# Performance work log

Hardware: AMD Instinct MI355X
Metric: run time of the kernel (lower is better)

## Reference

```python
import jax, jax.numpy as jnp
import numpy as np

N_NODES = 50000
N_EDGES = 800000
IN_DIM = 128
HID = 256
HEADS = 4
OUT_DIM = 128
NEG_SLOPE = 0.2


def gat_conv(x, src, dst, W, a_src, a_dst, b, heads, out_ch):
    """PyG-style GATConv: per-edge attention + segment softmax over dst."""
    N = x.shape[0]
    h = (x @ W).reshape(N, heads, out_ch)              # [N,H,C]
    alph_s = jnp.einsum('nhc,hc->nh', h, a_src)        # [N,H]
    alph_d = jnp.einsum('nhc,hc->nh', h, a_dst)        # [N,H]
    e = jax.nn.leaky_relu(alph_s[src] + alph_d[dst], NEG_SLOPE)  # [E,H]
    m = jax.lax.stop_gradient(jax.ops.segment_max(e, dst, num_segments=N))
    ex = jnp.exp(e - m[dst])
    s = jax.ops.segment_sum(ex, dst, num_segments=N)
    alpha = ex / (s[dst] + 1e-16)                      # [E,H]
    out = jax.ops.segment_sum(h[src] * alpha[:, :, None], dst, num_segments=N)
    return out.reshape(N, heads * out_ch) + b


def setup_inputs() -> dict:
    key = jax.random.key(0)
    ks = jax.random.split(key, 12)
    x = jax.random.normal(ks[0], (N_NODES, IN_DIM), dtype=jnp.float32)
    edge_index = jax.random.randint(ks[1], (2, N_EDGES), 0, N_NODES, dtype=jnp.int64)
    c1 = HID // HEADS  # 64
    sc1 = 1.0 / np.sqrt(IN_DIM)
    sc2 = 1.0 / np.sqrt(HID)
    W1 = jax.random.normal(ks[2], (IN_DIM, HID), dtype=jnp.float32) * sc1
    a1_src = jax.random.normal(ks[3], (HEADS, c1), dtype=jnp.float32) * sc1
    a1_dst = jax.random.normal(ks[4], (HEADS, c1), dtype=jnp.float32) * sc1
    b1 = jnp.zeros((HID,), dtype=jnp.float32)
    W2 = jax.random.normal(ks[5], (HID, OUT_DIM), dtype=jnp.float32) * sc2
    a2_src = jax.random.normal(ks[6], (1, OUT_DIM), dtype=jnp.float32) * sc2
    a2_dst = jax.random.normal(ks[7], (1, OUT_DIM), dtype=jnp.float32) * sc2
    b2 = jnp.zeros((OUT_DIM,), dtype=jnp.float32)
    return {"x": x, "edge_index": edge_index, "W1": W1, "a1_src": a1_src,
            "a1_dst": a1_dst, "b1": b1, "W2": W2, "a2_src": a2_src,
            "a2_dst": a2_dst, "b2": b2}


def reference(x, edge_index, W1, a1_src, a1_dst, b1, W2, a2_src, a2_dst, b2):
    N = x.shape[0]
    loops = jnp.arange(N, dtype=edge_index.dtype)
    # PyG default add_self_loops=True
    src = jnp.concatenate([edge_index[0], loops])
    dst = jnp.concatenate([edge_index[1], loops])
    h = jax.nn.relu(gat_conv(x, src, dst, W1, a1_src, a1_dst, b1, HEADS, HID // HEADS))
    # dropout is identity in eval mode
    return gat_conv(h, src, dst, W2, a2_src, a2_dst, b2, 1, OUT_DIM)
```

## Files before the change

kernel.cpp:

```cpp
#include <hip/hip_runtime.h>
#include <math.h>

#define NEG_SLOPE 0.2f
#define SLOTS 64
#define ECAP 63
#define NBMAX 391
#define BCAP 2432

typedef __attribute__((ext_vector_type(8))) short bf16x8;
typedef __attribute__((ext_vector_type(4))) float f32x4;
typedef __attribute__((ext_vector_type(2))) float f32x2;

__device__ __forceinline__ float lrelu(float t) {
    return t > 0.f ? t : NEG_SLOPE * t;
}
__device__ __forceinline__ unsigned short f2bf(float f) {
    unsigned u = __float_as_uint(f);
    unsigned r = (u + 0x7fff + ((u >> 16) & 1)) >> 16;
    return (unsigned short)r;
}
__device__ __forceinline__ f32x2 unpack2(unsigned v) {
    f32x2 r;
    r.x = __uint_as_float(v << 16);
    r.y = __uint_as_float(v & 0xffff0000u);
    return r;
}

__global__ void prep0(const float* __restrict__ W1, const float* __restrict__ a1s,
                      const float* __restrict__ a1d, float* __restrict__ vsd1,
                      const float* __restrict__ W2, const float* __restrict__ a2s,
                      const float* __restrict__ a2d, float* __restrict__ vsd2) {
    int i = blockIdx.x * 256 + threadIdx.x;
    if (i < 512) {
        int k = i >> 2, h = i & 3;
        float s = 0.f, d = 0.f;
        for (int c = 0; c < 64; c++) {
            float wv = W1[k * 256 + h * 64 + c];
            s += wv * a1s[h * 64 + c];
            d += wv * a1d[h * 64 + c];
        }
        vsd1[h * 128 + k] = s;
        vsd1[(4 + h) * 128 + k] = d;
    } else if (i < 768) {
        int j = i - 512;
        float s = 0.f, d = 0.f;
        for (int c = 0; c < 128; c++) {
            float wv = W2[j * 128 + c];
            s += wv * a2s[c];
            d += wv * a2d[c];
        }
        vsd2[j] = s;
        vsd2[256 + j] = d;
    }
}

#define EMIT(dd, ss)                                                     \
    {                                                                    \
        int bk_ = (dd) >> 7;                                             \
        int pos_ = atomicAdd(&cntS[bk_], 1);                             \
        if (pos_ < BCAP)                                                 \
            bin[(size_t)bk_ * BCAP + pos_] =                             \
                ((unsigned)((dd) & 127) << 16) | (unsigned)(ss);         \
    }

__global__ void mega(const int* __restrict__ src, const int* __restrict__ dst,
                     int* __restrict__ gcur, unsigned* __restrict__ bin,
                     const float* __restrict__ x, uint4* __restrict__ xb4,
                     const float* __restrict__ W1, unsigned short* __restrict__ W1t,
                     const float* __restrict__ W2, unsigned short* __restrict__ W2t,
                     const float* __restrict__ vsd1,
                     float* __restrict__ as1, float* __restrict__ ad1,
                     int E, int N, int nb, int bP1, int bC, int bW1, int bW2) {
    __shared__ float vs[1024];
    __shared__ int cntS[NBMAX];
    const int b = blockIdx.x, t = threadIdx.x;
    if (b < bP1) {
        for (int i = t; i < nb; i += 256) cntS[i] = 0;
        __syncthreads();
        const int4* s4p = (const int4*)src;
        const int4* d4p = (const int4*)dst;
        const int E4 = E >> 2;
        const int idx = b * 256 + t;
        const bool act = idx < E4;
        int4 sv = act ? s4p[idx] : (int4){0, 0, 0, 0};
        int4 dv = act ? d4p[idx] : (int4){0, 0, 0, 0};
        int exd = -1, exs = 0;
        if (b == 0 && (E4 << 2) + t < E) {
            exd = dst[(E4 << 2) + t];
            exs = src[(E4 << 2) + t];
        }
        if (act) {
            atomicAdd(&cntS[dv.x >> 7], 1);
            atomicAdd(&cntS[dv.y >> 7], 1);
            atomicAdd(&cntS[dv.z >> 7], 1);
            atomicAdd(&cntS[dv.w >> 7], 1);
        }
        if (exd >= 0) atomicAdd(&cntS[exd >> 7], 1);
        __syncthreads();
        for (int i = t; i < nb; i += 256) {
            int c = cntS[i];
            cntS[i] = c ? atomicAdd(&gcur[i], c) : 0;
        }
        __syncthreads();
        if (act) {
            EMIT(dv.x, sv.x);
            EMIT(dv.y, sv.y);
            EMIT(dv.z, sv.z);
            EMIT(dv.w, sv.w);
        }
        if (exd >= 0) EMIT(exd, exs);
    } else if (b < bC) {
        int i = (b - bP1) * 256 + t;
        if (i < N * 16) {
            const float4* x4 = (const float4*)x;
            float4 v0 = x4[2 * i], v1 = x4[2 * i + 1];
            uint4 o;
            o.x = (unsigned)f2bf(v0.x) | ((unsigned)f2bf(v0.y) << 16);
            o.y = (unsigned)f2bf(v0.z) | ((unsigned)f2bf(v0.w) << 16);
            o.z = (unsigned)f2bf(v1.x) | ((unsigned)f2bf(v1.y) << 16);
            o.w = (unsigned)f2bf(v1.z) | ((unsigned)f2bf(v1.w) << 16);
            xb4[i] = o;
        }
    } else if (b < bW1) {
        int i = (b - bC) * 256 + t;
        int n = i >> 7, k = i & 127;
        W1t[i] = f2bf(W1[k * 256 + n]);
    } else if (b < bW2) {
        int i = (b - bW1) * 256 + t;
        int n = i >> 8, k = i & 255;
        W2t[i] = f2bf(W2[k * 128 + n]);
    } else {
        for (int i = t; i < 1024; i += 256) vs[i] = vsd1[i];
        __syncthreads();
        int wave = t >> 6, lane = t & 63;
        int n = (b - bW2) * 4 + wave;
        if (n >= N) return;
        float acc[8];
#pragma unroll
        for (int j = 0; j < 8; j++) acc[j] = 0.f;
#pragma unroll
        for (int i = 0; i < 2; i++) {
            float xv = x[(size_t)n * 128 + i * 64 + lane];
#pragma unroll
            for (int j = 0; j < 8; j++) acc[j] += xv * vs[j * 128 + i * 64 + lane];
        }
#pragma unroll
        for (int off = 32; off > 0; off >>= 1) {
#pragma unroll
            for (int j = 0; j < 8; j++) acc[j] += __shfl_down(acc[j], off, 64);
        }
        if (lane == 0) {
#pragma unroll
            for (int h = 0; h < 4; h++) {
                as1[n * 4 + h] = acc[h];
                ad1[n * 4 + h] = acc[4 + h];
            }
        }
    }
}

__global__ __launch_bounds__(256) void build_csr(const int* __restrict__ gcur,
                                                 const unsigned* __restrict__ bin,
                                                 unsigned short* __restrict__ eSrc,
                                                 int* __restrict__ cursor) {
    __shared__ unsigned short slotS[128 * 64];
    __shared__ int lc[128];
    const int b = blockIdx.x, t = threadIdx.x;
    if (t < 128) lc[t] = 0;
    __syncthreads();
    int cnt = gcur[b];
    if (cnt > BCAP) cnt = BCAP;
    const unsigned* bb = bin + (size_t)b * BCAP;
    for (int i = t; i < cnt; i += 256) {
        unsigned e = bb[i];
        int dl = e >> 16;
        int p = atomicAdd(&lc[dl], 1);
        if (p < ECAP) slotS[(dl << 6) + p] = (unsigned short)(e & 0xffff);
    }
    __syncthreads();
    const uint4* sp = (const uint4*)slotS;
    uint4* dp = (uint4*)(eSrc + ((size_t)b << 13));
#pragma unroll
    for (int i = 0; i < 4; i++) dp[t + i * 256] = sp[t + i * 256];
    if (t < 128) cursor[(b << 7) + t] = lc[t];
}

__global__ __launch_bounds__(256) void gather_gemm1(
    const int* __restrict__ cursor, const unsigned short* __restrict__ eSrc,
    const unsigned short* __restrict__ Xb,
    const float* __restrict__ as_, const float* __restrict__ ad_,
    const unsigned short* __restrict__ W1t, const float* __restrict__ b1,
    const float* __restrict__ vsd2,
    unsigned short* __restrict__ out1b, float* __restrict__ as2,
    float* __restrict__ ad2, int N) {
    constexpr int LDT = 136;
    __shared__ __align__(16) short As[128 * LDT];
    __shared__ float4 alS[4][2][64];
    __shared__ int offS[4][2][64];
    const int t = threadIdx.x;
    const int wv = t >> 6, lane = t & 63;
    const int half = lane >> 5, hl = lane & 31;
    const int row0 = blockIdx.x * 32;

    for (int pass = 0; pass < 4; pass++) {
        const int ln = pass * 8 + wv * 2 + half;
        const int d = row0 + ln;
        const bool vn = d < N;
        int deg = 0;
        if (vn) { deg = cursor[d]; if (deg > ECAP) deg = ECAP; }
        float4 adv = make_float4(0.f, 0.f, 0.f, 0.f);
        if (vn) adv = ((const float4*)ad_)[d];

        const int beg = d << 6;
        const int j0 = hl, j1 = hl + 32;
        const bool a0 = vn && (j0 <= deg), a1 = vn && (j1 <= deg);
        int s0 = vn ? d : 0, s1 = vn ? d : 0;
        if (vn && j0 < deg) s0 = eSrc[beg + j0];
        if (vn && j1 < deg) s1 = eSrc[beg + j1];
        float4 q0 = make_float4(0.f, 0.f, 0.f, 0.f), q1 = q0;
        if (a0) q0 = ((const float4*)as_)[s0];
        if (a1) q1 = ((const float4*)as_)[s1];

        float qa0[4] = {q0.x, q0.y, q0.z, q0.w};
        float qa1[4] = {q1.x, q1.y, q1.z, q1.w};
        float ad4[4] = {adv.x, adv.y, adv.z, adv.w};
        float e0[4], e1[4], m[4];
#pragma unroll
        for (int h = 0; h < 4; h++) {
            e0[h] = a0 ? lrelu(qa0[h] + ad4[h]) : -1e30f;
            e1[h] = a1 ? lrelu(qa1[h] + ad4[h]) : -1e30f;
            m[h] = fmaxf(e0[h], e1[h]);
        }
#pragma unroll
        for (int off = 1; off < 32; off <<= 1)
#pragma unroll
            for (int h = 0; h < 4; h++) m[h] = fmaxf(m[h], __shfl_xor(m[h], off, 64));
        float x0[4], x1[4], sum[4];
#pragma unroll
        for (int h = 0; h < 4; h++) {
            x0[h] = a0 ? __expf(e0[h] - m[h]) : 0.f;
            x1[h] = a1 ? __expf(e1[h] - m[h]) : 0.f;
            sum[h] = x0[h] + x1[h];
        }
#pragma unroll
        for (int off = 1; off < 32; off <<= 1)
#pragma unroll
            for (int h = 0; h < 4; h++) sum[h] += __shfl_xor(sum[h], off, 64);
        float ri[4];
#pragma unroll
        for (int h = 0; h < 4; h++) ri[h] = 1.f / (sum[h] + 1e-16f);

        alS[wv][half][j0] = make_float4(x0[0] * ri[0], x0[1] * ri[1], x0[2] * ri[2], x0[3] * ri[3]);
        alS[wv][half][j1] = make_float4(x1[0] * ri[0], x1[1] * ri[1], x1[2] * ri[2], x1[3] * ri[3]);
        offS[wv][half][j0] = s0 << 8;
        offS[wv][half][j1] = s1 << 8;

        int rows = vn ? deg + 1 : 0;
        { int o = __shfl_xor(rows, 32, 64); rows = rows > o ? rows : o; }

        const char* Xc = (const char*)Xb;
        const int myoff = hl * 8;
        f32x2 acc[4][2];
#pragma unroll
        for (int h = 0; h < 4; h++) { acc[h][0] = (f32x2){0.f, 0.f}; acc[h][1] = (f32x2){0.f, 0.f}; }

        int j = 0;
        for (; j + 3 < rows; j += 4) {
            int o0 = offS[wv][half][j], o1 = offS[wv][half][j + 1];
            int o2 = offS[wv][half][j + 2], o3 = offS[wv][half][j + 3];
            uint2 v0 = *(const uint2*)(Xc + o0 + myoff);
            uint2 v1 = *(const uint2*)(Xc + o1 + myoff);
            uint2 v2 = *(const uint2*)(Xc + o2 + myoff);
            uint2 v3 = *(const uint2*)(Xc + o3 + myoff);
            float4 al0 = alS[wv][half][j];
            float4 al1 = alS[wv][half][j + 1];
            float4 al2 = alS[wv][half][j + 2];
            float4 al3 = alS[wv][half][j + 3];
            {
                f32x2 lo = unpack2(v0.x), hi = unpack2(v0.y);
                acc[0][0] += al0.x * lo; acc[0][1] += al0.x * hi;
                acc[1][0] += al0.y * lo; acc[1][1] += al0.y * hi;
                acc[2][0] += al0.z * lo; acc[2][1] += al0.z * hi;
                acc[3][0] += al0.w * lo; acc[3][1] += al0.w * hi;
            }
            {
                f32x2 lo = unpack2(v1.x), hi = unpack2(v1.y);
                acc[0][0] += al1.x * lo; acc[0][1] += al1.x * hi;
                acc[1][0] += al1.y * lo; acc[1][1] += al1.y * hi;
                acc[2][0] += al1.z * lo; acc[2][1] += al1.z * hi;
                acc[3][0] += al1.w * lo; acc[3][1] += al1.w * hi;
            }
            {
                f32x2 lo = unpack2(v2.x), hi = unpack2(v2.y);
                acc[0][0] += al2.x * lo; acc[0][1] += al2.x * hi;
                acc[1][0] += al2.y * lo; acc[1][1] += al2.y * hi;
                acc[2][0] += al2.z * lo; acc[2][1] += al2.z * hi;
                acc[3][0] += al2.w * lo; acc[3][1] += al2.w * hi;
            }
            {
                f32x2 lo = unpack2(v3.x), hi = unpack2(v3.y);
                acc[0][0] += al3.x * lo; acc[0][1] += al3.x * hi;
                acc[1][0] += al3.y * lo; acc[1][1] += al3.y * hi;
                acc[2][0] += al3.z * lo; acc[2][1] += al3.z * hi;
                acc[3][0] += al3.w * lo; acc[3][1] += al3.w * hi;
            }
        }
        for (; j < rows; j++) {
            int o0 = offS[wv][half][j];
            uint2 v0 = *(const uint2*)(Xc + o0 + myoff);
            float4 al0 = alS[wv][half][j];
            f32x2 lo = unpack2(v0.x), hi = unpack2(v0.y);
            acc[0][0] += al0.x * lo; acc[0][1] += al0.x * hi;
            acc[1][0] += al0.y * lo; acc[1][1] += al0.y * hi;
            acc[2][0] += al0.z * lo; acc[2][1] += al0.z * hi;
            acc[3][0] += al0.w * lo; acc[3][1] += al0.w * hi;
        }

        if (vn) {
#pragma unroll
            for (int h = 0; h < 4; h++) {
                uint2 pack;
                pack.x = (unsigned)f2bf(acc[h][0].x) | ((unsigned)f2bf(acc[h][0].y) << 16);
                pack.y = (unsigned)f2bf(acc[h][1].x) | ((unsigned)f2bf(acc[h][1].y) << 16);
                ((uint2*)&As[(h * 32 + ln) * LDT])[hl] = pack;
            }
        }
    }
    __syncthreads();

    const int h = wv;
    const short* Ah = &As[h * 32 * LDT];
    const unsigned short* Bh = W1t + (size_t)h * 64 * 128;
    const int l16 = lane & 15, quad = lane >> 4;

    f32x4 acc[2][4];
#pragma unroll
    for (int mt = 0; mt < 2; mt++)
#pragma unroll
        for (int nt = 0; nt < 4; nt++) acc[mt][nt] = (f32x4){0.f, 0.f, 0.f, 0.f};

#pragma unroll
    for (int ks = 0; ks < 4; ks++) {
        const int ko = ks * 32 + quad * 8;
        bf16x8 a0 = *(const bf16x8*)&Ah[l16 * LDT + ko];
        bf16x8 a1 = *(const bf16x8*)&Ah[(16 + l16) * LDT + ko];
#pragma unroll
        for (int nt = 0; nt < 4; nt++) {
            bf16x8 b = *(const bf16x8*)&Bh[(size_t)(nt * 16 + l16) * 128 + ko];
            acc[0][nt] = __builtin_amdgcn_mfma_f32_16x16x32_bf16(a0, b, acc[0][nt], 0, 0, 0);
            acc[1][nt] = __builtin_amdgcn_mfma_f32_16x16x32_bf16(a1, b, acc[1][nt], 0, 0, 0);
        }
    }

#pragma unroll
    for (int mt = 0; mt < 2; mt++) {
        int rb = row0 + mt * 16 + quad * 4;
#pragma unroll
        for (int rr = 0; rr < 4; rr++) {
            int row = rb + rr;
            float ps = 0.f, pd = 0.f;
#pragma unroll
            for (int nt = 0; nt < 4; nt++) {
                int cg = h * 64 + l16 + nt * 16;
                float rres = acc[mt][nt][rr] + b1[cg];
                rres = fmaxf(rres, 0.f);
                if (row < N) out1b[(size_t)row * 256 + cg] = f2bf(rres);
                ps += rres * vsd2[cg];
                pd += rres * vsd2[256 + cg];
            }
#pragma unroll
            for (int mask = 1; mask < 16; mask <<= 1) {
                ps += __shfl_xor(ps, mask, 64);
                pd += __shfl_xor(pd, mask, 64);
            }
            if (l16 == 0 && row < N) {
                atomicAdd(&as2[row], ps);
                atomicAdd(&ad2[row], pd);
            }
        }
    }
}

template <int K, int N>
__global__ __launch_bounds__(256) void gemm_mfma(const unsigned short* __restrict__ A,
                                                 const unsigned short* __restrict__ Bt,
                                                 unsigned short* __restrict__ Cb, int M) {
    constexpr int LDT = 72;
    __shared__ __align__(16) short As[128 * LDT];
    __shared__ __align__(16) short Bs[64 * LDT];
    const int t = threadIdx.x;
    const int wave = t >> 6, lane = t & 63;
    const int row0 = blockIdx.x * 128;
    const int n0 = blockIdx.y * 64;

    f32x4 acc[2][4];
#pragma unroll
    for (int mt = 0; mt < 2; mt++)
#pragma unroll
        for (int nt = 0; nt < 4; nt++) acc[mt][nt] = (f32x4){0.f, 0.f, 0.f, 0.f};

    const int r = t >> 3, c8 = (t & 7) * 8;
    for (int kc = 0; kc < K; kc += 64) {
        const unsigned short* srcA = A + (size_t)row0 * K + kc;
#pragma unroll
        for (int p = 0; p < 4; p++) {
            int rr = r + p * 32;
            *(bf16x8*)&As[rr * LDT + c8] = *(const bf16x8*)&srcA[(size_t)rr * K + c8];
        }
        const unsigned short* srcB = Bt + (size_t)n0 * K + kc;
#pragma unroll
        for (int p = 0; p < 2; p++) {
            int rr = r + p * 32;
            *(bf16x8*)&Bs[rr * LDT + c8] = *(const bf16x8*)&srcB[(size_t)rr * K + c8];
        }
        __syncthreads();

        const int mbase = wave * 32 + (lane & 15);
        const int quad = lane >> 4;
#pragma unroll
        for (int ks = 0; ks < 2; ks++) {
            int ko = ks * 32 + quad * 8;
            bf16x8 a0 = *(const bf16x8*)&As[mbase * LDT + ko];
            bf16x8 a1 = *(const bf16x8*)&As[(mbase + 16) * LDT + ko];
#pragma unroll
            for (int nt = 0; nt < 4; nt++) {
                bf16x8 b = *(const bf16x8*)&Bs[((lane & 15) + nt * 16) * LDT + ko];
                acc[0][nt] = __builtin_amdgcn_mfma_f32_16x16x32_bf16(a0, b, acc[0][nt], 0, 0, 0);
                acc[1][nt] = __builtin_amdgcn_mfma_f32_16x16x32_bf16(a1, b, acc[1][nt], 0, 0, 0);
            }
        }
        __syncthreads();
    }

    const int colb = n0 + (lane & 15);
    const int rquad = (lane >> 4) * 4;
#pragma unroll
    for (int mt = 0; mt < 2; mt++) {
        int rb = row0 + wave * 32 + mt * 16 + rquad;
#pragma unroll
        for (int nt = 0; nt < 4; nt++) {
#pragma unroll
            for (int rr2 = 0; rr2 < 4; rr2++) {
                int row = rb + rr2;
                if (row < M) Cb[(size_t)row * N + colb + nt * 16] = f2bf(acc[mt][nt][rr2]);
            }
        }
    }
}

__global__ __launch_bounds__(256) void fused_gather2(
    const int* __restrict__ cursor, const unsigned short* __restrict__ eSrc,
    const unsigned short* __restrict__ Hb,
    const float* __restrict__ as_, const float* __restrict__ ad_,
    const float* __restrict__ b2, float* __restrict__ out, int N) {
    const int wv = threadIdx.x >> 6, lane = threadIdx.x & 63;
    const int half = lane >> 5, hl = lane & 31;
    const int d = blockIdx.x * 8 + wv * 2 + half;

    __shared__ float alS[4][2][64];
    __shared__ int offS[4][2][64];

    const bool vn = d < N;
    int deg = 0;
    if (vn) { deg = cursor[d]; if (deg > ECAP) deg = ECAP; }
    const float adv = vn ? ad_[d] : 0.f;

    const int beg = d << 6;
    const int j0 = hl, j1 = hl + 32;
    const bool a0 = vn && (j0 <= deg), a1 = vn && (j1 <= deg);
    int s0 = vn ? d : 0, s1 = vn ? d : 0;
    if (vn && j0 < deg) s0 = eSrc[beg + j0];
    if (vn && j1 < deg) s1 = eSrc[beg + j1];
    float e0 = a0 ? lrelu(as_[s0] + adv) : -1e30f;
    float e1 = a1 ? lrelu(as_[s1] + adv) : -1e30f;
    float m = fmaxf(e0, e1);
#pragma unroll
    for (int off = 1; off < 32; off <<= 1) m = fmaxf(m, __shfl_xor(m, off, 64));
    float x0 = a0 ? __expf(e0 - m) : 0.f;
    float x1 = a1 ? __expf(e1 - m) : 0.f;
    float sum = x0 + x1;
#pragma unroll
    for (int off = 1; off < 32; off <<= 1) sum += __shfl_xor(sum, off, 64);
    float ri = 1.f / (sum + 1e-16f);

    alS[wv][half][j0] = x0 * ri;
    alS[wv][half][j1] = x1 * ri;
    offS[wv][half][j0] = s0 << 8;
    offS[wv][half][j1] = s1 << 8;

    int rows = vn ? deg + 1 : 0;
    { int o = __shfl_xor(rows, 32, 64); rows = rows > o ? rows : o; }

    const char* Hc = (const char*)Hb;
    const int myoff = hl * 8;
    f32x2 acc0 = (f32x2){0.f, 0.f}, acc1 = (f32x2){0.f, 0.f};

    int j = 0;
    for (; j + 3 < rows; j += 4) {
        int o0 = offS[wv][half][j], o1 = offS[wv][half][j + 1];
        int o2 = offS[wv][half][j + 2], o3 = offS[wv][half][j + 3];
        uint2 v0 = *(const uint2*)(Hc + o0 + myoff);
        uint2 v1 = *(const uint2*)(Hc + o1 + myoff);
        uint2 v2 = *(const uint2*)(Hc + o2 + myoff);
        uint2 v3 = *(const uint2*)(Hc + o3 + myoff);
        float b0 = alS[wv][half][j], b1v = alS[wv][half][j + 1];
        float b2v = alS[wv][half][j + 2], b3 = alS[wv][half][j + 3];
        acc0 += b0 * unpack2(v0.x); acc1 += b0 * unpack2(v0.y);
        acc0 += b1v * unpack2(v1.x); acc1 += b1v * unpack2(v1.y);
        acc0 += b2v * unpack2(v2.x); acc1 += b2v * unpack2(v2.y);
        acc0 += b3 * unpack2(v3.x); acc1 += b3 * unpack2(v3.y);
    }
    for (; j < rows; j++) {
        int o0 = offS[wv][half][j];
        uint2 v0 = *(const uint2*)(Hc + o0 + myoff);
        float b0 = alS[wv][half][j];
        acc0 += b0 * unpack2(v0.x); acc1 += b0 * unpack2(v0.y);
    }

    if (vn) {
        float4 bb = ((const float4*)b2)[hl];
        float4 o;
        o.x = acc0.x + bb.x;
        o.y = acc0.y + bb.y;
        o.z = acc1.x + bb.z;
        o.w = acc1.y + bb.w;
        ((float4*)(out + (size_t)d * 128))[hl] = o;
    }
}

extern "C" void kernel_launch(void* const* d_in, const int* in_sizes, int n_in,
                              void* d_out, int out_size, void* d_ws, size_t ws_size,
                              hipStream_t stream) {
    const float* x   = (const float*)d_in[0];
    const int*   ei  = (const int*)d_in[1];
    const float* W1  = (const float*)d_in[2];
    const float* a1s = (const float*)d_in[3];
    const float* a1d = (const float*)d_in[4];
    const float* b1  = (const float*)d_in[5];
    const float* W2  = (const float*)d_in[6];
    const float* a2s = (const float*)d_in[7];
    const float* a2d = (const float*)d_in[8];
    const float* b2  = (const float*)d_in[9];

    const int N = in_sizes[0] / 128;
    const int E = in_sizes[1] / 2;
    const int* srcIdx = ei;
    const int* dstIdx = ei + E;
    float* out = (float*)d_out;

    const int MT = (N + 127) / 128;
    const int M_pad = MT * 128;
    const int nb = (N + 127) >> 7;

    char* w = (char*)d_ws;
    unsigned short* x_bf  = (unsigned short*)w; w += (size_t)N * 128 * 2;
    unsigned short* out1b = (unsigned short*)w; w += (size_t)M_pad * 256 * 2;
    unsigned short* h2b   = (unsigned short*)w; w += (size_t)N * 128 * 2;
    unsigned short* W1t   = (unsigned short*)w; w += (size_t)128 * 256 * 2;
    unsigned short* W2t   = (unsigned short*)w; w += (size_t)256 * 128 * 2;
    float* vsd1 = (float*)w; w += (size_t)128 * 8 * 4;
    float* vsd2 = (float*)w; w += (size_t)256 * 2 * 4;
    float* as1  = (float*)w; w += (size_t)N * 4 * 4;
    float* ad1  = (float*)w; w += (size_t)N * 4 * 4;
    float* as2  = (float*)w; w += (size_t)N * 4;
    float* ad2  = (float*)w; w += (size_t)N * 4;
    int* cursor = (int*)w;  w += (size_t)M_pad * 4;
    unsigned short* eSrc = (unsigned short*)w; w += (size_t)M_pad * SLOTS * 2;
    int* gcur = (int*)w; w += (size_t)nb * 4;
    unsigned* bin = (unsigned*)out1b;

    hipMemsetAsync(gcur, 0, (size_t)nb * 4, stream);
    hipMemsetAsync(as2, 0, (size_t)N * 4, stream);
    hipMemsetAsync(ad2, 0, (size_t)N * 4, stream);

    prep0<<<3, 256, 0, stream>>>(W1, a1s, a1d, vsd1, W2, a2s, a2d, vsd2);

    {
        const int bP1 = (E / 4 + 255) / 256;
        const int nC  = (N * 16 + 255) / 256;
        const int bC  = bP1 + nC;
        const int bW1 = bC + 128;
        const int bW2 = bW1 + 128;
        const int nG  = (N + 3) / 4;
        mega<<<bW2 + nG, 256, 0, stream>>>(srcIdx, dstIdx, gcur, bin,
                                           x, (uint4*)x_bf, W1, W1t, W2, W2t,
                                           vsd1, as1, ad1, E, N, nb, bP1, bC, bW1, bW2);
    }

    build_csr<<<nb, 256, 0, stream>>>(gcur, bin, eSrc, cursor);

    gather_gemm1<<<(N + 31) / 32, 256, 0, stream>>>(cursor, eSrc, x_bf, as1, ad1,
                                                    W1t, b1, vsd2, out1b, as2, ad2, N);

    gemm_mfma<256, 128><<<dim3(MT, 2), 256, 0, stream>>>(out1b, W2t, h2b, N);
    fused_gather2<<<(N + 7) / 8, 256, 0, stream>>>(cursor, eSrc, h2b, as2, ad2, b2, out, N);
}
```

Before: 294.8 us.

## Split layer-1 gather from GEMM and fuse both dense GEMMs into one kernel

The layer-1 gather+GEMM kernel is split. A lightweight gather kernel now writes per-head aggregated features to a head-major workspace. A new gemm12 kernel then chains the W1 GEMM, bias+ReLU, the layer-2 attention projections and the W2 GEMM per 64-row tile, keeping the hidden activations in LDS. This removes the out1b round trip, the separate W2 GEMM launch, the atomics and the memsets for as2/ad2, and gives the gather smaller blocks with no 35KB LDS, which should raise occupancy. In exchange the aggregated features (4×N×128 bf16) now make a global round trip, and gemm12 reads W1/W2 slices directly from global memory.

```diff
diff --git a/kernel.cpp b/kernel.cpp
--- a/kernel.cpp
+++ b/kernel.cpp
@@ -185,265 +185,232 @@
     if (t < 128) cursor[(b << 7) + t] = lc[t];
 }
 
-__global__ __launch_bounds__(256) void gather_gemm1(
+__global__ __launch_bounds__(256) void fused_gather1(
     const int* __restrict__ cursor, const unsigned short* __restrict__ eSrc,
     const unsigned short* __restrict__ Xb,
     const float* __restrict__ as_, const float* __restrict__ ad_,
-    const unsigned short* __restrict__ W1t, const float* __restrict__ b1,
-    const float* __restrict__ vsd2,
-    unsigned short* __restrict__ out1b, float* __restrict__ as2,
-    float* __restrict__ ad2, int N) {
-    constexpr int LDT = 136;
-    __shared__ __align__(16) short As[128 * LDT];
+    unsigned short* __restrict__ agg, int N, int Mpad) {
+    const int wv = threadIdx.x >> 6, lane = threadIdx.x & 63;
+    const int half = lane >> 5, hl = lane & 31;
+    const int d = blockIdx.x * 8 + wv * 2 + half;
+
     __shared__ float4 alS[4][2][64];
     __shared__ int offS[4][2][64];
-    const int t = threadIdx.x;
-    const int wv = t >> 6, lane = t & 63;
-    const int half = lane >> 5, hl = lane & 31;
-    const int row0 = blockIdx.x * 32;
-
-    for (int pass = 0; pass < 4; pass++) {
-        const int ln = pass * 8 + wv * 2 + half;
-        const int d = row0 + ln;
-        const bool vn = d < N;
-        int deg = 0;
-        if (vn) { deg = cursor[d]; if (deg > ECAP) deg = ECAP; }
-        float4 adv = make_float4(0.f, 0.f, 0.f, 0.f);
-        if (vn) adv = ((const float4*)ad_)[d];
-
-        const int beg = d << 6;
-        const int j0 = hl, j1 = hl + 32;
-        const bool a0 = vn && (j0 <= deg), a1 = vn && (j1 <= deg);
-        int s0 = vn ? d : 0, s1 = vn ? d : 0;
-        if (vn && j0 < deg) s0 = eSrc[beg + j0];
-        if (vn && j1 < deg) s1 = eSrc[beg + j1];
-        float4 q0 = make_float4(0.f, 0.f, 0.f, 0.f), q1 = q0;
-        if (a0) q0 = ((const float4*)as_)[s0];
-        if (a1) q1 = ((const float4*)as_)[s1];
-
-        float qa0[4] = {q0.x, q0.y, q0.z, q0.w};
-        float qa1[4] = {q1.x, q1.y, q1.z, q1.w};
-        float ad4[4] = {adv.x, adv.y, adv.z, adv.w};
-        float e0[4], e1[4], m[4];
-#pragma unroll
-        for (int h = 0; h < 4; h++) {
-            e0[h] = a0 ? lrelu(qa0[h] + ad4[h]) : -1e30f;
-            e1[h] = a1 ? lrelu(qa1[h] + ad4[h]) : -1e30f;
-            m[h] = fmaxf(e0[h], e1[h]);
-        }
-#pragma unroll
-        for (int off = 1; off < 32; off <<= 1)
-#pragma unroll
-            for (int h = 0; h < 4; h++) m[h] = fmaxf(m[h], __shfl_xor(m[h], off, 64));
-        float x0[4], x1[4], sum[4];
-#pragma unroll
-        for (int h = 0; h < 4; h++) {
-            x0[h] = a0 ? __expf(e0[h] - m[h]) : 0.f;
-            x1[h] = a1 ? __expf(e1[h] - m[h]) : 0.f;
-            sum[h] = x0[h] + x1[h];
-        }
-#pragma unroll
-        for (int off = 1; off < 32; off <<= 1)
-#pragma unroll
-            for (int h = 0; h < 4; h++) sum[h] += __shfl_xor(sum[h], off, 64);
-        float ri[4];
-#pragma unroll
-        for (int h = 0; h < 4; h++) ri[h] = 1.f / (sum[h] + 1e-16f);
-
-        alS[wv][half][j0] = make_float4(x0[0] * ri[0], x0[1] * ri[1], x0[2] * ri[2], x0[3] * ri[3]);
-        alS[wv][half][j1] = make_float4(x1[0] * ri[0], x1[1] * ri[1], x1[2] * ri[2], x1[3] * ri[3]);
-        offS[wv][half][j0] = s0 << 8;
-        offS[wv][half][j1] = s1 << 8;
-
-        int rows = vn ? deg + 1 : 0;
-        { int o = __shfl_xor(rows, 32, 64); rows = rows > o ? rows : o; }
-
-        const char* Xc = (const char*)Xb;
-        const int myoff = hl * 8;
-        f32x2 acc[4][2];
-#pragma unroll
-        for (int h = 0; h < 4; h++) { acc[h][0] = (f32x2){0.f, 0.f}; acc[h][1] = (f32x2){0.f, 0.f}; }
-
-        int j = 0;
-        for (; j + 3 < rows; j += 4) {
-            int o0 = offS[wv][half][j], o1 = offS[wv][half][j + 1];
-            int o2 = offS[wv][half][j + 2], o3 = offS[wv][half][j + 3];
-            uint2 v0 = *(const uint2*)(Xc + o0 + myoff);
-            uint2 v1 = *(const uint2*)(Xc + o1 + myoff);
-            uint2 v2 = *(const uint2*)(Xc + o2 + myoff);
-            uint2 v3 = *(const uint2*)(Xc + o3 + myoff);
-            float4 al0 = alS[wv][half][j];
-            float4 al1 = alS[wv][half][j + 1];
-            float4 al2 = alS[wv][half][j + 2];
-            float4 al3 = alS[wv][half][j + 3];
-            {
-                f32x2 lo = unpack2(v0.x), hi = unpack2(v0.y);
-                acc[0][0] += al0.x * lo; acc[0][1] += al0.x * hi;
-                acc[1][0] += al0.y * lo; acc[1][1] += al0.y * hi;
-                acc[2][0] += al0.z * lo; acc[2][1] += al0.z * hi;
-                acc[3][0] += al0.w * lo; acc[3][1] += al0.w * hi;
-            }
-            {
-                f32x2 lo = unpack2(v1.x), hi = unpack2(v1.y);
-                acc[0][0] += al1.x * lo; acc[0][1] += al1.x * hi;
-                acc[1][0] += al1.y * lo; acc[1][1] += al1.y * hi;
-                acc[2][0] += al1.z * lo; acc[2][1] += al1.z * hi;
-                acc[3][0] += al1.w * lo; acc[3][1] += al1.w * hi;
-            }
-            {
-                f32x2 lo = unpack2(v2.x), hi = unpack2(v2.y);
-                acc[0][0] += al2.x * lo; acc[0][1] += al2.x * hi;
-                acc[1][0] += al2.y * lo; acc[1][1] += al2.y * hi;
-                acc[2][0] += al2.z * lo; acc[2][1] += al2.z * hi;
-                acc[3][0] += al2.w * lo; acc[3][1] += al2.w * hi;
-            }
-            {
-                f32x2 lo = unpack2(v3.x), hi = unpack2(v3.y);
-                acc[0][0] += al3.x * lo; acc[0][1] += al3.x * hi;
-                acc[1][0] += al3.y * lo; acc[1][1] += al3.y * hi;
-                acc[2][0] += al3.z * lo; acc[2][1] += al3.z * hi;
-                acc[3][0] += al3.w * lo; acc[3][1] += al3.w * hi;
-            }
-        }
-        for (; j < rows; j++) {
-            int o0 = offS[wv][half][j];
-            uint2 v0 = *(const uint2*)(Xc + o0 + myoff);
-            float4 al0 = alS[wv][half][j];
+
+    const bool vn = d < N;
+    int deg = 0;
+    if (vn) { deg = cursor[d]; if (deg > ECAP) deg = ECAP; }
+    float4 adv = make_float4(0.f, 0.f, 0.f, 0.f);
+    if (vn) adv = ((const float4*)ad_)[d];
+
+    const int beg = d << 6;
+    const int j0 = hl, j1 = hl + 32;
+    const bool a0 = vn && (j0 <= deg), a1 = vn && (j1 <= deg);
+    int s0 = vn ? d : 0, s1 = vn ? d : 0;
+    if (vn && j0 < deg) s0 = eSrc[beg + j0];
+    if (vn && j1 < deg) s1 = eSrc[beg + j1];
+    float4 q0 = make_float4(0.f, 0.f, 0.f, 0.f), q1 = q0;
+    if (a0) q0 = ((const float4*)as_)[s0];
+    if (a1) q1 = ((const float4*)as_)[s1];
+
+    float qa0[4] = {q0.x, q0.y, q0.z, q0.w};
+    float qa1[4] = {q1.x, q1.y, q1.z, q1.w};
+    float ad4[4] = {adv.x, adv.y, adv.z, adv.w};
+    float e0[4], e1[4], m[4];
+#pragma unroll
+    for (int h = 0; h < 4; h++) {
+        e0[h] = a0 ? lrelu(qa0[h] + ad4[h]) : -1e30f;
+        e1[h] = a1 ? lrelu(qa1[h] + ad4[h]) : -1e30f;
+        m[h] = fmaxf(e0[h], e1[h]);
+    }
+#pragma unroll
+    for (int off = 1; off < 32; off <<= 1)
+#pragma unroll
+        for (int h = 0; h < 4; h++) m[h] = fmaxf(m[h], __shfl_xor(m[h], off, 64));
+    float x0[4], x1[4], sum[4];
+#pragma unroll
+    for (int h = 0; h < 4; h++) {
+        x0[h] = a0 ? __expf(e0[h] - m[h]) : 0.f;
+        x1[h] = a1 ? __expf(e1[h] - m[h]) : 0.f;
+        sum[h] = x0[h] + x1[h];
+    }
+#pragma unroll
+    for (int off = 1; off < 32; off <<= 1)
+#pragma unroll
+        for (int h = 0; h < 4; h++) sum[h] += __shfl_xor(sum[h], off, 64);
+    float ri[4];
+#pragma unroll
+    for (int h = 0; h < 4; h++) ri[h] = 1.f / (sum[h] + 1e-16f);
+
+    alS[wv][half][j0] = make_float4(x0[0] * ri[0], x0[1] * ri[1], x0[2] * ri[2], x0[3] * ri[3]);
+    alS[wv][half][j1] = make_float4(x1[0] * ri[0], x1[1] * ri[1], x1[2] * ri[2], x1[3] * ri[3]);
+    offS[wv][half][j0] = s0 << 8;
+    offS[wv][half][j1] = s1 << 8;
+
+    int rows = vn ? deg + 1 : 0;
+    { int o = __shfl_xor(rows, 32, 64); rows = rows > o ? rows : o; }
+
+    const char* Xc = (const char*)Xb;
+    const int myoff = hl * 8;
+    f32x2 acc[4][2];
+#pragma unroll
+    for (int h = 0; h < 4; h++) { acc[h][0] = (f32x2){0.f, 0.f}; acc[h][1] = (f32x2){0.f, 0.f}; }
+
+    int j = 0;
+    for (; j + 3 < rows; j += 4) {
+        int o0 = offS[wv][half][j], o1 = offS[wv][half][j + 1];
+        int o2 = offS[wv][half][j + 2], o3 = offS[wv][half][j + 3];
+        uint2 v0 = *(const uint2*)(Xc + o0 + myoff);
+        uint2 v1 = *(const uint2*)(Xc + o1 + myoff);
+        uint2 v2 = *(const uint2*)(Xc + o2 + myoff);
+        uint2 v3 = *(const uint2*)(Xc + o3 + myoff);
+        float4 al0 = alS[wv][half][j];
+        float4 al1 = alS[wv][half][j + 1];
+        float4 al2 = alS[wv][half][j + 2];
+        float4 al3 = alS[wv][half][j + 3];
+        {
             f32x2 lo = unpack2(v0.x), hi = unpack2(v0.y);
             acc[0][0] += al0.x * lo; acc[0][1] += al0.x * hi;
             acc[1][0] += al0.y * lo; acc[1][1] += al0.y * hi;
             acc[2][0] += al0.z * lo; acc[2][1] += al0.z * hi;
             acc[3][0] += al0.w * lo; acc[3][1] += al0.w * hi;
         }
-
-        if (vn) {
-#pragma unroll
-            for (int h = 0; h < 4; h++) {
-                uint2 pack;
-                pack.x = (unsigned)f2bf(acc[h][0].x) | ((unsigned)f2bf(acc[h][0].y) << 16);
-                pack.y = (unsigned)f2bf(acc[h][1].x) | ((unsigned)f2bf(acc[h][1].y) << 16);
-                ((uint2*)&As[(h * 32 + ln) * LDT])[hl] = pack;
+        {
+            f32x2 lo = unpack2(v1.x), hi = unpack2(v1.y);
+            acc[0][0] += al1.x * lo; acc[0][1] += al1.x * hi;
+            acc[1][0] += al1.y * lo; acc[1][1] += al1.y * hi;
+            acc[2][0] += al1.z * lo; acc[2][1] += al1.z * hi;
+            acc[3][0] += al1.w * lo; acc[3][1] += al1.w * hi;
+        }
+        {
+            f32x2 lo = unpack2(v2.x), hi = unpack2(v2.y);
+            acc[0][0] += al2.x * lo; acc[0][1] += al2.x * hi;
+            acc[1][0] += al2.y * lo; acc[1][1] += al2.y * hi;
+            acc[2][0] += al2.z * lo; acc[2][1] += al2.z * hi;
+            acc[3][0] += al2.w * lo; acc[3][1] += al2.w * hi;
+        }
+        {
+            f32x2 lo = unpack2(v3.x), hi = unpack2(v3.y);
+            acc[0][0] += al3.x * lo; acc[0][1] += al3.x * hi;
+            acc[1][0] += al3.y * lo; acc[1][1] += al3.y * hi;
+            acc[2][0] += al3.z * lo; acc[2][1] += al3.z * hi;
+            acc[3][0] += al3.w * lo; acc[3][1] += al3.w * hi;
+        }
+    }
+    for (; j < rows; j++) {
+        int o0 = offS[wv][half][j];
+        uint2 v0 = *(const uint2*)(Xc + o0 + myoff);
+        float4 al0 = alS[wv][half][j];
+        f32x2 lo = unpack2(v0.x), hi = unpack2(v0.y);
+        acc[0][0] += al0.x * lo; acc[0][1] += al0.x * hi;
+        acc[1][0] += al0.y * lo; acc[1][1] += al0.y * hi;
+        acc[2][0] += al0.z * lo; acc[2][1] += al0.z * hi;
+        acc[3][0] += al0.w * lo; acc[3][1] += al0.w * hi;
+    }
+
+    if (vn) {
+#pragma unroll
+        for (int h = 0; h < 4; h++) {
+            uint2 pack;
+            pack.x = (unsigned)f2bf(acc[h][0].x) | ((unsigned)f2bf(acc[h][0].y) << 16);
+            pack.y = (unsigned)f2bf(acc[h][1].x) | ((unsigned)f2bf(acc[h][1].y) << 16);
+            ((uint2*)(agg + ((size_t)h * Mpad + d) * 128))[hl] = pack;
+        }
+    }
+}
+
+__global__ __launch_bounds__(256) void gemm12(
+    const unsigned short* __restrict__ agg, const unsigned short* __restrict__ W1t,
+    const float* __restrict__ b1, const unsigned short* __restrict__ W2t,
+    const float* __restrict__ vsd2, unsigned short* __restrict__ h2b,
+    float* __restrict__ as2, float* __restrict__ ad2, int N, int Mpad) {
+    constexpr int LDA = 136;
+    constexpr int LDC = 72;
+    __shared__ __align__(16) short As[64 * LDA];
+    __shared__ __align__(16) short Cb[64 * LDC];
+    const int t = threadIdx.x;
+    const int w = t >> 6, lane = t & 63;
+    const int l16 = lane & 15, quad = lane >> 4;
+    const int row0 = blockIdx.x * 64;
+    const int rs = t >> 4, cs = (t & 15) * 8;
+
+    f32x4 acc2[8];
+#pragma unroll
+    for (int nt = 0; nt < 8; nt++) acc2[nt] = (f32x4){0.f, 0.f, 0.f, 0.f};
+    float ps[4] = {0.f, 0.f, 0.f, 0.f}, pd[4] = {0.f, 0.f, 0.f, 0.f};
+
+    for (int h = 0; h < 4; h++) {
+        const unsigned short* srcA = agg + ((size_t)h * Mpad + row0) * 128;
+#pragma unroll
+        for (int p = 0; p < 4; p++) {
+            int rr = rs + p * 16;
+            *(bf16x8*)&As[rr * LDA + cs] = *(const bf16x8*)&srcA[(size_t)rr * 128 + cs];
+        }
+        __syncthreads();
+
+        f32x4 acc1[4];
+#pragma unroll
+        for (int nt = 0; nt < 4; nt++) acc1[nt] = (f32x4){0.f, 0.f, 0.f, 0.f};
+        const unsigned short* Bh = W1t + (size_t)h * 64 * 128;
+#pragma unroll
+        for (int ks = 0; ks < 4; ks++) {
+            const int ko = ks * 32 + quad * 8;
+            bf16x8 a = *(const bf16x8*)&As[(w * 16 + l16) * LDA + ko];
+#pragma unroll
+            for (int nt = 0; nt < 4; nt++) {
+                bf16x8 b = *(const bf16x8*)&Bh[(size_t)(nt * 16 + l16) * 128 + ko];
+                acc1[nt] = __builtin_amdgcn_mfma_f32_16x16x32_bf16(a, b, acc1[nt], 0, 0, 0);
             }
         }
-    }
-    __syncthreads();
-
-    const int h = wv;
-    const short* Ah = &As[h * 32 * LDT];
-    const unsigned short* Bh = W1t + (size_t)h * 64 * 128;
-    const int l16 = lane & 15, quad = lane >> 4;
-
-    f32x4 acc[2][4];
-#pragma unroll
-    for (int mt = 0; mt < 2; mt++)
-#pragma unroll
-        for (int nt = 0; nt < 4; nt++) acc[mt][nt] = (f32x4){0.f, 0.f, 0.f, 0.f};
-
-#pragma unroll
-    for (int ks = 0; ks < 4; ks++) {
-        const int ko = ks * 32 + quad * 8;
-        bf16x8 a0 = *(const bf16x8*)&Ah[l16 * LDT + ko];
-        bf16x8 a1 = *(const bf16x8*)&Ah[(16 + l16) * LDT + ko];
+
 #pragma unroll
         for (int nt = 0; nt < 4; nt++) {
-            bf16x8 b = *(const bf16x8*)&Bh[(size_t)(nt * 16 + l16) * 128 + ko];
-            acc[0][nt] = __builtin_amdgcn_mfma_f32_16x16x32_bf16(a0, b, acc[0][nt], 0, 0, 0);
-            acc[1][nt] = __builtin_amdgcn_mfma_f32_16x16x32_bf16(a1, b, acc[1][nt], 0, 0, 0);
-        }
-    }
-
-#pragma unroll
-    for (int mt = 0; mt < 2; mt++) {
-        int rb = row0 + mt * 16 + quad * 4;
+            const int cg = h * 64 + nt * 16 + l16;
+            const float bb = b1[cg];
+            const float v2s = vsd2[cg], v2d = vsd2[256 + cg];
+#pragma unroll
+            for (int rr = 0; rr < 4; rr++) {
+                float v = fmaxf(acc1[nt][rr] + bb, 0.f);
+                Cb[(w * 16 + quad * 4 + rr) * LDC + nt * 16 + l16] = (short)f2bf(v);
+                ps[rr] += v * v2s;
+                pd[rr] += v * v2d;
+            }
+        }
+        __syncthreads();
+
+#pragma unroll
+        for (int ks = 0; ks < 2; ks++) {
+            const int ko = ks * 32 + quad * 8;
+            bf16x8 a = *(const bf16x8*)&Cb[(w * 16 + l16) * LDC + ko];
+#pragma unroll
+            for (int nt = 0; nt < 8; nt++) {
+                bf16x8 b = *(const bf16x8*)&W2t[(size_t)(nt * 16 + l16) * 256 + h * 64 + ko];
+                acc2[nt] = __builtin_amdgcn_mfma_f32_16x16x32_bf16(a, b, acc2[nt], 0, 0, 0);
+            }
+        }
+        __syncthreads();
+    }
+
+#pragma unroll
+    for (int nt = 0; nt < 8; nt++) {
 #pragma unroll
         for (int rr = 0; rr < 4; rr++) {
-            int row = rb + rr;
-            float ps = 0.f, pd = 0.f;
-#pragma unroll
-            for (int nt = 0; nt < 4; nt++) {
-                int cg = h * 64 + l16 + nt * 16;
-                float rres = acc[mt][nt][rr] + b1[cg];
-                rres = fmaxf(rres, 0.f);
-                if (row < N) out1b[(size_t)row * 256 + cg] = f2bf(rres);
-                ps += rres * vsd2[cg];
-                pd += rres * vsd2[256 + cg];
-            }
-#pragma unroll
-            for (int mask = 1; mask < 16; mask <<= 1) {
-                ps += __shfl_xor(ps, mask, 64);
-                pd += __shfl_xor(pd, mask, 64);
-            }
-            if (l16 == 0 && row < N) {
-                atomicAdd(&as2[row], ps);
-                atomicAdd(&ad2[row], pd);
-            }
-        }
-    }
-}
-
-template <int K, int N>
-__global__ __launch_bounds__(256) void gemm_mfma(const unsigned short* __restrict__ A,
-                                                 const unsigned short* __restrict__ Bt,
-                                                 unsigned short* __restrict__ Cb, int M) {
-    constexpr int LDT = 72;
-    __shared__ __align__(16) short As[128 * LDT];
-    __shared__ __align__(16) short Bs[64 * LDT];
-    const int t = threadIdx.x;
-    const int wave = t >> 6, lane = t & 63;
-    const int row0 = blockIdx.x * 128;
-    const int n0 = blockIdx.y * 64;
-
-    f32x4 acc[2][4];
-#pragma unroll
-    for (int mt = 0; mt < 2; mt++)
-#pragma unroll
-        for (int nt = 0; nt < 4; nt++) acc[mt][nt] = (f32x4){0.f, 0.f, 0.f, 0.f};
-
-    const int r = t >> 3, c8 = (t & 7) * 8;
-    for (int kc = 0; kc < K; kc += 64) {
-        const unsigned short* srcA = A + (size_t)row0 * K + kc;
-#pragma unroll
-        for (int p = 0; p < 4; p++) {
-            int rr = r + p * 32;
-            *(bf16x8*)&As[rr * LDT + c8] = *(const bf16x8*)&srcA[(size_t)rr * K + c8];
-        }
-        const unsigned short* srcB = Bt + (size_t)n0 * K + kc;
-#pragma unroll
-        for (int p = 0; p < 2; p++) {
-            int rr = r + p * 32;
-            *(bf16x8*)&Bs[rr * LDT + c8] = *(const bf16x8*)&srcB[(size_t)rr * K + c8];
-        }
-        __syncthreads();
-
-        const int mbase = wave * 32 + (lane & 15);
-        const int quad = lane >> 4;
-#pragma unroll
-        for (int ks = 0; ks < 2; ks++) {
-            int ko = ks * 32 + quad * 8;
-            bf16x8 a0 = *(const bf16x8*)&As[mbase * LDT + ko];
-            bf16x8 a1 = *(const bf16x8*)&As[(mbase + 16) * LDT + ko];
-#pragma unroll
-            for (int nt = 0; nt < 4; nt++) {
-                bf16x8 b = *(const bf16x8*)&Bs[((lane & 15) + nt * 16) * LDT + ko];
-                acc[0][nt] = __builtin_amdgcn_mfma_f32_16x16x32_bf16(a0, b, acc[0][nt], 0, 0, 0);
-                acc[1][nt] = __builtin_amdgcn_mfma_f32_16x16x32_bf16(a1, b, acc[1][nt], 0, 0, 0);
-            }
-        }
-        __syncthreads();
-    }
-
-    const int colb = n0 + (lane & 15);
-    const int rquad = (lane >> 4) * 4;
-#pragma unroll
-    for (int mt = 0; mt < 2; mt++) {
-        int rb = row0 + wave * 32 + mt * 16 + rquad;
-#pragma unroll
-        for (int nt = 0; nt < 4; nt++) {
-#pragma unroll
-            for (int rr2 = 0; rr2 < 4; rr2++) {
-                int row = rb + rr2;
-                if (row < M) Cb[(size_t)row * N + colb + nt * 16] = f2bf(acc[mt][nt][rr2]);
-            }
+            const int row = row0 + w * 16 + quad * 4 + rr;
+            if (row < N) h2b[(size_t)row * 128 + nt * 16 + l16] = f2bf(acc2[nt][rr]);
+        }
+    }
+#pragma unroll
+    for (int rr = 0; rr < 4; rr++) {
+        float p = ps[rr], q = pd[rr];
+#pragma unroll
+        for (int mask = 1; mask < 16; mask <<= 1) {
+            p += __shfl_xor(p, mask, 64);
+            q += __shfl_xor(q, mask, 64);
+        }
+        const int row = row0 + w * 16 + quad * 4 + rr;
+        if (l16 == 0 && row < N) {
+            as2[row] = p;
+            ad2[row] = q;
         }
     }
 }
@@ -554,7 +521,7 @@
 
     char* w = (char*)d_ws;
     unsigned short* x_bf  = (unsigned short*)w; w += (size_t)N * 128 * 2;
-    unsigned short* out1b = (unsigned short*)w; w += (size_t)M_pad * 256 * 2;
+    unsigned short* agg   = (unsigned short*)w; w += (size_t)4 * M_pad * 128 * 2;
     unsigned short* h2b   = (unsigned short*)w; w += (size_t)N * 128 * 2;
     unsigned short* W1t   = (unsigned short*)w; w += (size_t)128 * 256 * 2;
     unsigned short* W2t   = (unsigned short*)w; w += (size_t)256 * 128 * 2;
@@ -567,11 +534,9 @@
     int* cursor = (int*)w;  w += (size_t)M_pad * 4;
     unsigned short* eSrc = (unsigned short*)w; w += (size_t)M_pad * SLOTS * 2;
     int* gcur = (int*)w; w += (size_t)nb * 4;
-    unsigned* bin = (unsigned*)out1b;
+    unsigned* bin = (unsigned*)agg;
 
     hipMemsetAsync(gcur, 0, (size_t)nb * 4, stream);
-    hipMemsetAsync(as2, 0, (size_t)N * 4, stream);
-    hipMemsetAsync(ad2, 0, (size_t)N * 4, stream);
 
     prep0<<<3, 256, 0, stream>>>(W1, a1s, a1d, vsd1, W2, a2s, a2d, vsd2);
 
@@ -589,9 +554,9 @@
 
     build_csr<<<nb, 256, 0, stream>>>(gcur, bin, eSrc, cursor);
 
-    gather_gemm1<<<(N + 31) / 32, 256, 0, stream>>>(cursor, eSrc, x_bf, as1, ad1,
-                                                    W1t, b1, vsd2, out1b, as2, ad2, N);
-
-    gemm_mfma<256, 128><<<dim3(MT, 2), 256, 0, stream>>>(out1b, W2t, h2b, N);
+    fused_gather1<<<(N + 7) / 8, 256, 0, stream>>>(cursor, eSrc, x_bf, as1, ad1, agg, N, M_pad);
+
+    gemm12<<<(N + 63) / 64, 256, 0, stream>>>(agg, W1t, b1, W2t, vsd2, h2b, as2, ad2, N, M_pad);
+
     fused_gather2<<<(N + 7) / 8, 256, 0, stream>>>(cursor, eSrc, h2b, as2, ad2, b2, out, N);
 }
```

After: 304.6 us. +3.3%, slower.
